# Optimization experiments

Hardware: AMD Instinct MI355X
Metric: run time of the kernel (lower is better)

## Reference

```python
import jax, jax.numpy as jnp
import numpy as np

N, E, F_IN = 50000, 1_600_000, 256
HID, HEADS, NCLS = 8, 8, 16  # conv1: 8 heads x 8 dims (concat=64); conv2: 1 head -> 16 classes


def setup_inputs() -> dict:
    key = jax.random.key(0)
    ks = jax.random.split(key, 11)
    x = jax.random.normal(ks[0], (N, F_IN), dtype=jnp.float32)
    edge_index = jax.random.randint(ks[1], (2, E), 0, N, dtype=jnp.int32)
    s1 = 1.0 / np.sqrt(F_IN)
    W1 = jax.random.normal(ks[2], (F_IN, HEADS * HID), jnp.float32) * s1
    a_src1 = jax.random.normal(ks[3], (HEADS, HID), jnp.float32) * 0.1
    a_dst1 = jax.random.normal(ks[4], (HEADS, HID), jnp.float32) * 0.1
    b1 = jnp.zeros((HEADS * HID,), jnp.float32)
    s2 = 1.0 / np.sqrt(HEADS * HID)
    W2 = jax.random.normal(ks[5], (HEADS * HID, NCLS), jnp.float32) * s2
    a_src2 = jax.random.normal(ks[6], (1, NCLS), jnp.float32) * 0.1
    a_dst2 = jax.random.normal(ks[7], (1, NCLS), jnp.float32) * 0.1
    b2 = jnp.zeros((NCLS,), jnp.float32)
    return {"x": x, "edge_index": edge_index, "W1": W1, "a_src1": a_src1,
            "a_dst1": a_dst1, "b1": b1, "W2": W2, "a_src2": a_src2,
            "a_dst2": a_dst2, "b2": b2}


def _gat_conv(x, W, a_src, a_dst, bias, src, dst, n, heads, ch, concat):
    # per-head linear transform: [n, heads, ch]
    h = (x @ W).reshape(n, heads, ch)
    # additive attention logits per node, per head
    al_s = jnp.einsum('nhc,hc->nh', h, a_src)
    al_d = jnp.einsum('nhc,hc->nh', h, a_dst)
    e = jax.nn.leaky_relu(al_s[src] + al_d[dst], 0.2)  # [E_tot, heads]
    # segment softmax grouped by destination node (self-loops guarantee non-empty segments)
    m = jax.ops.segment_max(e, dst, num_segments=n)
    ex = jnp.exp(e - m[dst])
    den = jax.ops.segment_sum(ex, dst, num_segments=n)
    alpha = ex / den[dst]  # [E_tot, heads]
    # scatter-aggregate weighted neighbor features
    out = jax.ops.segment_sum(h[src] * alpha[:, :, None], dst, num_segments=n)
    out = out.reshape(n, heads * ch) if concat else out.mean(axis=1)
    return out + bias


def reference(x, edge_index, W1, a_src1, a_dst1, b1, W2, a_src2, a_dst2, b2):
    # add self-loops (PyG GATConv default)
    loops = jnp.arange(N, dtype=edge_index.dtype)
    src = jnp.concatenate([edge_index[0], loops])
    dst = jnp.concatenate([edge_index[1], loops])
    h = _gat_conv(x, W1, a_src1, a_dst1, b1, src, dst, N, HEADS, HID, True)
    h = jax.nn.elu(h)
    out = _gat_conv(h, W2, a_src2, a_dst2, b2, src, dst, N, 1, NCLS, False)
    return jax.nn.log_softmax(out, axis=1)
```

## Files before the change

### kernel.cpp

```cpp
#include <hip/hip_runtime.h>
#include <hip/hip_fp16.h>

#define NN   50000
#define FIN  256
#define C1   64
#define NH   8
#define NC   16
#define NE   1600000
#define NTOT (NE + NN)

#define CH   256
#define EPC  ((NTOT + CH - 1) / CH)
#define NCB  392
#define GB1  ((NN + 63) / 64)

typedef _Float16 half8 __attribute__((ext_vector_type(8)));
typedef _Float16 half4 __attribute__((ext_vector_type(4)));
typedef float f32x4 __attribute__((ext_vector_type(4)));

#define OFF_H1H   0
#define OFF_G1H   1600000
#define OFF_STAGE 3200000
#define OFF_H2H   3200000
#define OFF_ALS2  3600000
#define OFF_ALD2  3650000
#define OFF_ALS1  6400000
#define OFF_ALD1  6800000
#define OFF_HM    7200000
#define OFF_BASEK 7300352
#define OFF_BBASE 7400704
#define OFF_OFFS  7401600
#define OFF_SRC   7451700
#define OFF_W1T   9101700

__global__ __launch_bounds__(256) void k_wcvt(const float* __restrict__ W1,
                                              _Float16* __restrict__ w1t) {
    int t = blockIdx.x * 256 + threadIdx.x;
    int c = t >> 8, k = t & 255;
    w1t[t] = (_Float16)W1[k * C1 + c];
}

__global__ __launch_bounds__(256) void k_g1rh(const float* __restrict__ x,
                                              const _Float16* __restrict__ w1t,
                                              const float* __restrict__ as1,
                                              const float* __restrict__ ad1,
                                              _Float16* __restrict__ h1h,
                                              float* __restrict__ als,
                                              float* __restrict__ ald,
                                              const int* __restrict__ ei,
                                              int* __restrict__ H) {
    __shared__ _Float16 wsT[64][264];
    __shared__ int lh[NCB];
    const int tid = threadIdx.x;

    if (blockIdx.x >= GB1) {
        int k = blockIdx.x - GB1;
        for (int i = tid; i < NCB; i += 256) lh[i] = 0;
        __syncthreads();
        int e0 = k * EPC, e1 = min(e0 + EPC, NTOT);
        for (int e = e0 + tid; e < e1; e += 256) {
            int d = (e < NE) ? ei[NE + e] : (e - NE);
            atomicAdd(&lh[d >> 7], 1);
        }
        __syncthreads();
        for (int i = tid; i < NCB; i += 256) H[k * NCB + i] = lh[i];
        return;
    }

    const int r0 = blockIdx.x * 64;
    #pragma unroll
    for (int j = 0; j < 8; ++j) {
        int idx = tid * 8 + j * 2048;
        int c = idx >> 8, ko = idx & 255;
        *(half8*)(&wsT[c][ko]) = *(const half8*)(&w1t[idx]);
    }
    __syncthreads();

    const int lane = tid & 63;
    const int wv   = tid >> 6;
    const int colb = lane & 15;
    const int rgrp = lane >> 4;
    const int arow = r0 + wv * 16 + colb;
    const bool arv = arow < NN;
    f32x4 acc[4] = {};
    #pragma unroll
    for (int s = 0; s < 8; ++s) {
        float4 v0 = make_float4(0.f,0.f,0.f,0.f), v1 = v0;
        if (arv) {
            const float4* xp = (const float4*)(&x[(size_t)arow * FIN + s * 32 + rgrp * 8]);
            v0 = xp[0]; v1 = xp[1];
        }
        half8 a;
        a[0]=(_Float16)v0.x; a[1]=(_Float16)v0.y; a[2]=(_Float16)v0.z; a[3]=(_Float16)v0.w;
        a[4]=(_Float16)v1.x; a[5]=(_Float16)v1.y; a[6]=(_Float16)v1.z; a[7]=(_Float16)v1.w;
        #pragma unroll
        for (int ct = 0; ct < 4; ++ct) {
            half8 b = *(half8*)(&wsT[ct * 16 + colb][s * 32 + rgrp * 8]);
            acc[ct] = __builtin_amdgcn_mfma_f32_16x16x32_f16(a, b, acc[ct], 0, 0, 0);
        }
    }
    __syncthreads();
    _Float16 (*hstore)[72] = (_Float16(*)[72])wsT;
    #pragma unroll
    for (int j = 0; j < 4; ++j) {
        int row = wv * 16 + rgrp * 4 + j;
        #pragma unroll
        for (int ct = 0; ct < 4; ++ct)
            hstore[row][ct * 16 + colb] = (_Float16)acc[ct][j];
    }
    __syncthreads();
    {
        int row = tid >> 2, seg = tid & 3;
        int grow = r0 + row;
        if (grow < NN) {
            half8 h0 = *(half8*)(&hstore[row][seg * 16]);
            half8 h1v = *(half8*)(&hstore[row][seg * 16 + 8]);
            *(half8*)(&h1h[(size_t)grow * C1 + seg * 16])     = h0;
            *(half8*)(&h1h[(size_t)grow * C1 + seg * 16 + 8]) = h1v;
            float ps0 = 0.f, pd0 = 0.f, ps1 = 0.f, pd1 = 0.f;
            #pragma unroll
            for (int u = 0; u < 8; ++u) {
                float a0 = (float)h0[u], a1 = (float)h1v[u];
                ps0 += a0 * as1[seg * 16 + u];
                pd0 += a0 * ad1[seg * 16 + u];
                ps1 += a1 * as1[seg * 16 + 8 + u];
                pd1 += a1 * ad1[seg * 16 + 8 + u];
            }
            als[grow * NH + seg * 2]     = ps0;
            als[grow * NH + seg * 2 + 1] = ps1;
            ald[grow * NH + seg * 2]     = pd0;
            ald[grow * NH + seg * 2 + 1] = pd1;
        }
    }
}

__global__ __launch_bounds__(256) void k_rsA(const int* __restrict__ H,
                                             int* __restrict__ basek,
                                             int* __restrict__ btot) {
    __shared__ int sc[CH];
    int b = blockIdx.x, t = threadIdx.x;
    int v = H[t * NCB + b];
    sc[t] = v;
    __syncthreads();
    for (int s = 1; s < CH; s <<= 1) {
        int u = (t >= s) ? sc[t - s] : 0;
        __syncthreads();
        sc[t] += u;
        __syncthreads();
    }
    basek[b * CH + t] = sc[t] - v;
    if (t == CH - 1) btot[b] = sc[t];
}

__global__ __launch_bounds__(512) void k_rsB(const int* __restrict__ btot,
                                             int* __restrict__ bbase,
                                             int* __restrict__ offs) {
    __shared__ int sc[512];
    int t = threadIdx.x;
    int v = (t < NCB) ? btot[t] : 0;
    sc[t] = v;
    __syncthreads();
    for (int s = 1; s < 512; s <<= 1) {
        int u = (t >= s) ? sc[t - s] : 0;
        __syncthreads();
        sc[t] += u;
        __syncthreads();
    }
    if (t < NCB) bbase[t] = sc[t] - v;
    if (t == NCB - 1) bbase[NCB] = sc[t];
    if (t == 0) offs[NN] = NTOT;
}

__global__ __launch_bounds__(256) void k_rscatter(const int* __restrict__ ei,
                                                  const int* __restrict__ basek,
                                                  const int* __restrict__ bbase,
                                                  int* __restrict__ stage) {
    __shared__ int lcur[NCB];
    int k = blockIdx.x;
    for (int i = threadIdx.x; i < NCB; i += 256)
        lcur[i] = bbase[i] + basek[i * CH + k];
    __syncthreads();
    int e0 = k * EPC, e1 = min(e0 + EPC, NTOT);
    for (int e = e0 + threadIdx.x; e < e1; e += 256) {
        int s, d;
        if (e < NE) { s = ei[e]; d = ei[NE + e]; }
        else        { s = e - NE; d = s; }
        int pos = atomicAdd(&lcur[d >> 7], 1);
        stage[pos] = (s << 7) | (d & 127);
    }
}

__global__ __launch_bounds__(256) void k_fsort(const int* __restrict__ stage,
                                               const int* __restrict__ bbase,
                                               int* __restrict__ offs,
                                               int* __restrict__ ssrc) {
    __shared__ int lc[128];
    __shared__ int ls[128];
    __shared__ int lcur[128];
    int b = blockIdx.x, t = threadIdx.x;
    int base = bbase[b];
    int n = bbase[b + 1] - base;
    if (t < 128) lc[t] = 0;
    __syncthreads();
    const int* sp = &stage[base];
    for (int i = t; i < n; i += 256) atomicAdd(&lc[sp[i] & 127], 1);
    __syncthreads();
    int v = (t < 128) ? lc[t] : 0;
    if (t < 128) ls[t] = v;
    __syncthreads();
    for (int s = 1; s < 128; s <<= 1) {
        int u = (t >= s && t < 128) ? ls[t - s] : 0;
        __syncthreads();
        if (t < 128) ls[t] += u;
        __syncthreads();
    }
    if (t < 128) {
        int excl = ls[t] - v;
        int d = b * 128 + t;
        if (d < NN) offs[d] = base + excl;
        lcur[t] = base + excl;
    }
    __syncthreads();
    for (int i = t; i < n; i += 256) {
        int u = sp[i];
        int pos = atomicAdd(&lcur[u & 127], 1);
        ssrc[pos] = u >> 7;
    }
}

__global__ __launch_bounds__(256) void k_agg1(const int* __restrict__ offs,
                                              const int* __restrict__ src,
                                              const __half* __restrict__ h1h,
                                              const float* __restrict__ als,
                                              const float* __restrict__ ald,
                                              const float* __restrict__ b1,
                                              _Float16* __restrict__ g1h) {
    int d = blockIdx.x * 4 + (threadIdx.x >> 6);
    if (d >= NN) return;
    const int l  = threadIdx.x & 63;
    const int q  = l >> 4, lc = l & 15;
    const int hg = lc >> 1;
    const int sub = l >> 3, hw = l & 7;
    const int lane_a = (q << 3) | hg;
    const int lane_b = lane_a + 32;
    const unsigned coff = (unsigned)lc * 8u;
    const unsigned hoff = (unsigned)hw * 4u;
    const char* h1b = (const char*)h1h;
    const char* alb = (const char*)als;
    int beg = offs[d], end = offs[d + 1];
    float aldv = ald[d * NH + hw];
    f32x4 acc = {0.f, 0.f, 0.f, 0.f};
    float wsum = 0.f;

    int r = beg;
    int e0 = r + sub, e1 = e0 + 8;
    int s0 = src[e0 < end ? e0 : end - 1];
    int s1 = src[e1 < end ? e1 : end - 1];
    {
        float lg0 = *(const float*)(alb + ((unsigned)s0 * 32u + hoff)) + aldv;
        float lg1 = *(const float*)(alb + ((unsigned)s1 * 32u + hoff)) + aldv;
        lg0 = lg0 > 0.f ? lg0 : 0.2f * lg0;
        lg1 = lg1 > 0.f ? lg1 : 0.2f * lg1;
        s0 = e0 < end ? s0 : s0;
        float w0t = e0 < end ? __expf(lg0) : 0.f;
        float w1t = e1 < end ? __expf(lg1) : 0.f;
        acc[0] = acc[0];
        float w0 = w0t, w1 = w1t;
        while (r < end) {
            int rn = r + 16;
            bool more = rn < end;
            int s0n = s0, s1n = s1;
            if (more) {
                int f0 = rn + sub, f1 = f0 + 8;
                s0n = src[f0 < end ? f0 : end - 1];
                s1n = src[f1 < end ? f1 : end - 1];
            }
            wsum += w0 + w1;
            #pragma unroll
            for (int i = 0; i < 4; ++i) {
                int srcl = (i & 1) ? lane_b : lane_a;
                int sv   = __shfl((i < 2) ? s0 : s1, srcl);
                float wv = __shfl((i < 2) ? w0 : w1, srcl);
                half4 hv = *(const half4*)(h1b + ((unsigned)sv * 128u + coff));
                acc[0] += wv * (float)hv[0];
                acc[1] += wv * (float)hv[1];
                acc[2] += wv * (float)hv[2];
                acc[3] += wv * (float)hv[3];
            }
            if (more) {
                float g0 = *(const float*)(alb + ((unsigned)s0n * 32u + hoff)) + aldv;
                float g1 = *(const float*)(alb + ((unsigned)s1n * 32u + hoff)) + aldv;
                g0 = g0 > 0.f ? g0 : 0.2f * g0;
                g1 = g1 > 0.f ? g1 : 0.2f * g1;
                w0 = (rn + sub) < end ? __expf(g0) : 0.f;
                w1 = (rn + 8 + sub) < end ? __expf(g1) : 0.f;
            }
            s0 = s0n; s1 = s1n; r = rn;
        }
    }
    #pragma unroll
    for (int k = 0; k < 4; ++k) {
        acc[k] += __shfl_xor(acc[k], 16);
        acc[k] += __shfl_xor(acc[k], 32);
    }
    wsum += __shfl_xor(wsum, 8);
    wsum += __shfl_xor(wsum, 16);
    wsum += __shfl_xor(wsum, 32);
    float den = __shfl(wsum, hg);
    if (q == 0) {
        half4 gv;
        #pragma unroll
        for (int k = 0; k < 4; ++k) {
            float o = acc[k] / den + b1[4 * lc + k];
            o = o > 0.f ? o : (__expf(o) - 1.f);
            gv[k] = (_Float16)o;
        }
        *(half4*)(&g1h[(size_t)d * C1 + 4 * lc]) = gv;
    }
}

__global__ __launch_bounds__(256) void k_gemm2(const _Float16* __restrict__ g1h,
                                               const float* __restrict__ W2,
                                               const float* __restrict__ as2,
                                               const float* __restrict__ ad2,
                                               _Float16* __restrict__ h2h,
                                               float* __restrict__ als2,
                                               float* __restrict__ ald2) {
    __shared__ float w2s[C1][17];
    __shared__ _Float16 hact[16][C1 + 8];
    int tid = threadIdx.x;
    for (int i = tid; i < C1 * NC; i += 256) w2s[i >> 4][i & 15] = W2[i];
    int ln = tid >> 4, j = tid & 15;
    int n = blockIdx.x * 16 + ln;
    if (n < NN)
        *(half4*)(&hact[ln][j * 4]) = *(const half4*)(&g1h[(size_t)n * C1 + j * 4]);
    __syncthreads();
    if (n >= NN) return;
    float sum = 0.f;
    #pragma unroll
    for (int c = 0; c < C1; ++c) sum += (float)hact[ln][c] * w2s[c][j];
    h2h[(size_t)n * NC + j] = (_Float16)sum;
    float ps = sum * as2[j], pd = sum * ad2[j];
    #pragma unroll
    for (int w = 1; w < 16; w <<= 1) {
        ps += __shfl_xor(ps, w);
        pd += __shfl_xor(pd, w);
    }
    if (j == 0) { als2[n] = ps; ald2[n] = pd; }
}

__global__ __launch_bounds__(256) void k_agg2(const int* __restrict__ offs,
                                              const int* __restrict__ src,
                                              const _Float16* __restrict__ h2h,
                                              const float* __restrict__ als2,
                                              const float* __restrict__ ald2,
                                              const float* __restrict__ b2,
                                              float* __restrict__ out) {
    int d = blockIdx.x * 16 + (threadIdx.x >> 4);
    if (d >= NN) return;
    int c = threadIdx.x & 15;
    const unsigned coff = (unsigned)c * 2u;
    const char* h2b = (const char*)h2h;
    const char* alb = (const char*)als2;
    int beg = offs[d], end = offs[d + 1];
    float aldv = ald2[d];
    float acc = 0.f, den = 0.f;
    for (int r = beg; r < end; r += 8) {
        int ss[8];
        float ww[8];
        #pragma unroll
        for (int i = 0; i < 8; ++i) {
            int e = r + i;
            ss[i] = src[e < end ? e : end - 1];
        }
        #pragma unroll
        for (int i = 0; i < 8; ++i) {
            float lg = *(const float*)(alb + (unsigned)ss[i] * 4u) + aldv;
            lg = lg > 0.f ? lg : 0.2f * lg;
            ww[i] = (r + i) < end ? __expf(lg) : 0.f;
        }
        #pragma unroll
        for (int i = 0; i < 8; ++i) {
            float hv = (float)*(const _Float16*)(h2b + ((unsigned)ss[i] * 32u + coff));
            acc += ww[i] * hv;
            den += ww[i];
        }
    }
    float o = acc / den + b2[c];
    float m = o;
    #pragma unroll
    for (int w = 1; w < 16; w <<= 1) m = fmaxf(m, __shfl_xor(m, w));
    float ex = __expf(o - m);
    float sm = ex;
    #pragma unroll
    for (int w = 1; w < 16; w <<= 1) sm += __shfl_xor(sm, w);
    out[(size_t)d * NC + c] = o - m - __logf(sm);
}

extern "C" void kernel_launch(void* const* d_in, const int* in_sizes, int n_in,
                              void* d_out, int out_size, void* d_ws, size_t ws_size,
                              hipStream_t stream) {
    const float* x   = (const float*)d_in[0];
    const int*   ei  = (const int*)  d_in[1];
    const float* W1  = (const float*)d_in[2];
    const float* as1 = (const float*)d_in[3];
    const float* ad1 = (const float*)d_in[4];
    const float* b1  = (const float*)d_in[5];
    const float* W2  = (const float*)d_in[6];
    const float* as2 = (const float*)d_in[7];
    const float* ad2 = (const float*)d_in[8];
    const float* b2  = (const float*)d_in[9];
    float* ws  = (float*)d_ws;
    float* out = (float*)d_out;

    _Float16*  h1h  = (_Float16*)(ws + OFF_H1H);
    _Float16*  g1h  = (_Float16*)(ws + OFF_G1H);
    _Float16*  h2h  = (_Float16*)(ws + OFF_H2H);
    _Float16*  w1t  = (_Float16*)(ws + OFF_W1T);
    float* als1 = ws + OFF_ALS1;
    float* ald1 = ws + OFF_ALD1;
    float* als2 = ws + OFF_ALS2;
    float* ald2 = ws + OFF_ALD2;
    int* H      = (int*)(ws + OFF_HM);
    int* basek  = (int*)(ws + OFF_BASEK);
    int* bbase  = (int*)(ws + OFF_BBASE);
    int* btot   = (int*)(ws + OFF_BBASE) + 400;
    int* offs   = (int*)(ws + OFF_OFFS);
    int* ssrc   = (int*)(ws + OFF_SRC);
    int* stage  = (int*)(ws + OFF_STAGE);

    k_wcvt    <<<64,             256, 0, stream>>>(W1, w1t);
    k_g1rh    <<<GB1 + CH,       256, 0, stream>>>(x, w1t, as1, ad1, h1h, als1, ald1, ei, H);
    k_rsA     <<<NCB,            256, 0, stream>>>(H, basek, btot);
    k_rsB     <<<1,              512, 0, stream>>>(btot, bbase, offs);
    k_rscatter<<<CH,             256, 0, stream>>>(ei, basek, bbase, stage);
    k_fsort   <<<NCB,            256, 0, stream>>>(stage, bbase, offs, ssrc);
    k_agg1    <<<(NN + 3) / 4,   256, 0, stream>>>(offs, ssrc, (const __half*)h1h, als1, ald1, b1, g1h);
    k_gemm2   <<<(NN + 15) / 16, 256, 0, stream>>>(g1h, W2, as2, ad2, h2h, als2, ald2);
    k_agg2    <<<(NN + 15) / 16, 256, 0, stream>>>(offs, ssrc, h2h, als2, ald2, b2, out);
}
```

Measured before the change: 137.4 us.

## Drop W1 convert and rsB kernels, widen sort buckets, restructure aggregation kernels

Removes the separate W1 fp16 transpose kernel by converting W1 inline when loading shared memory in the GEMM, and folds the single-block bucket-total scan into the scatter and fine-sort kernels, which each recompute it. Bucket width doubles from 128 to 256 nodes, halving the bucket count. Layer-1 aggregation now gives each lane its own edge slot with half8 feature loads instead of shuffle-based broadcasting and software prefetch. Layer-2 aggregation uses a 64-lane wave per node with half4 loads and float4 output stores. Fewer launches and wider memory ops are traded for redundant scans and uncoalesced W1 reads per GEMM block.

```diff
diff --git a/kernel.cpp b/kernel.cpp
--- a/kernel.cpp
+++ b/kernel.cpp
@@ -11,7 +11,7 @@
 
 #define CH   256
 #define EPC  ((NTOT + CH - 1) / CH)
-#define NCB  392
+#define NCB  196
 #define GB1  ((NN + 63) / 64)
 
 typedef _Float16 half8 __attribute__((ext_vector_type(8)));
@@ -28,20 +28,12 @@
 #define OFF_ALD1  6800000
 #define OFF_HM    7200000
 #define OFF_BASEK 7300352
-#define OFF_BBASE 7400704
+#define OFF_BTOT  7400704
 #define OFF_OFFS  7401600
 #define OFF_SRC   7451700
-#define OFF_W1T   9101700
-
-__global__ __launch_bounds__(256) void k_wcvt(const float* __restrict__ W1,
-                                              _Float16* __restrict__ w1t) {
-    int t = blockIdx.x * 256 + threadIdx.x;
-    int c = t >> 8, k = t & 255;
-    w1t[t] = (_Float16)W1[k * C1 + c];
-}
 
 __global__ __launch_bounds__(256) void k_g1rh(const float* __restrict__ x,
-                                              const _Float16* __restrict__ w1t,
+                                              const float* __restrict__ W1,
                                               const float* __restrict__ as1,
                                               const float* __restrict__ ad1,
                                               _Float16* __restrict__ h1h,
@@ -60,7 +52,7 @@
         int e0 = k * EPC, e1 = min(e0 + EPC, NTOT);
         for (int e = e0 + tid; e < e1; e += 256) {
             int d = (e < NE) ? ei[NE + e] : (e - NE);
-            atomicAdd(&lh[d >> 7], 1);
+            atomicAdd(&lh[d >> 8], 1);
         }
         __syncthreads();
         for (int i = tid; i < NCB; i += 256) H[k * NCB + i] = lh[i];
@@ -68,11 +60,17 @@
     }
 
     const int r0 = blockIdx.x * 64;
-    #pragma unroll
-    for (int j = 0; j < 8; ++j) {
-        int idx = tid * 8 + j * 2048;
-        int c = idx >> 8, ko = idx & 255;
-        *(half8*)(&wsT[c][ko]) = *(const half8*)(&w1t[idx]);
+    {
+        int c = tid & 63, kb = tid >> 6;
+        #pragma unroll
+        for (int j = 0; j < 8; ++j) {
+            int k8 = kb + 4 * j;
+            half8 hv;
+            #pragma unroll
+            for (int u = 0; u < 8; ++u)
+                hv[u] = (_Float16)W1[(size_t)(k8 * 8 + u) * C1 + c];
+            *(half8*)(&wsT[c][k8 * 8]) = hv;
+        }
     }
     __syncthreads();
 
@@ -152,170 +150,140 @@
     if (t == CH - 1) btot[b] = sc[t];
 }
 
-__global__ __launch_bounds__(512) void k_rsB(const int* __restrict__ btot,
-                                             int* __restrict__ bbase,
-                                             int* __restrict__ offs) {
-    __shared__ int sc[512];
-    int t = threadIdx.x;
+__global__ __launch_bounds__(256) void k_rscatter(const int* __restrict__ ei,
+                                                  const int* __restrict__ basek,
+                                                  const int* __restrict__ btot,
+                                                  int* __restrict__ stage) {
+    __shared__ int sc[256];
+    __shared__ int lcur[NCB];
+    int k = blockIdx.x, t = threadIdx.x;
     int v = (t < NCB) ? btot[t] : 0;
     sc[t] = v;
     __syncthreads();
-    for (int s = 1; s < 512; s <<= 1) {
+    for (int s = 1; s < 256; s <<= 1) {
         int u = (t >= s) ? sc[t - s] : 0;
         __syncthreads();
         sc[t] += u;
         __syncthreads();
     }
-    if (t < NCB) bbase[t] = sc[t] - v;
-    if (t == NCB - 1) bbase[NCB] = sc[t];
-    if (t == 0) offs[NN] = NTOT;
-}
-
-__global__ __launch_bounds__(256) void k_rscatter(const int* __restrict__ ei,
-                                                  const int* __restrict__ basek,
-                                                  const int* __restrict__ bbase,
-                                                  int* __restrict__ stage) {
-    __shared__ int lcur[NCB];
-    int k = blockIdx.x;
-    for (int i = threadIdx.x; i < NCB; i += 256)
-        lcur[i] = bbase[i] + basek[i * CH + k];
+    if (t < NCB) lcur[t] = (sc[t] - v) + basek[t * CH + k];
     __syncthreads();
     int e0 = k * EPC, e1 = min(e0 + EPC, NTOT);
-    for (int e = e0 + threadIdx.x; e < e1; e += 256) {
+    for (int e = e0 + t; e < e1; e += 256) {
         int s, d;
         if (e < NE) { s = ei[e]; d = ei[NE + e]; }
         else        { s = e - NE; d = s; }
-        int pos = atomicAdd(&lcur[d >> 7], 1);
-        stage[pos] = (s << 7) | (d & 127);
+        int pos = atomicAdd(&lcur[d >> 8], 1);
+        stage[pos] = (s << 8) | (d & 255);
     }
 }
 
 __global__ __launch_bounds__(256) void k_fsort(const int* __restrict__ stage,
-                                               const int* __restrict__ bbase,
+                                               const int* __restrict__ btot,
                                                int* __restrict__ offs,
                                                int* __restrict__ ssrc) {
-    __shared__ int lc[128];
-    __shared__ int ls[128];
-    __shared__ int lcur[128];
+    __shared__ int sc[256];
+    __shared__ int lc[256];
+    __shared__ int ls[256];
+    __shared__ int lcur[256];
+    __shared__ int bb[2];
     int b = blockIdx.x, t = threadIdx.x;
-    int base = bbase[b];
-    int n = bbase[b + 1] - base;
-    if (t < 128) lc[t] = 0;
-    __syncthreads();
+    int v = (t < NCB) ? btot[t] : 0;
+    sc[t] = v;
+    __syncthreads();
+    for (int s = 1; s < 256; s <<= 1) {
+        int u = (t >= s) ? sc[t - s] : 0;
+        __syncthreads();
+        sc[t] += u;
+        __syncthreads();
+    }
+    if (t == b) bb[0] = sc[t] - v;
+    if (t == b) bb[1] = sc[t];
+    if (b == 0 && t == 0) offs[NN] = NTOT;
+    lc[t] = 0;
+    __syncthreads();
+    int base = bb[0];
+    int n = bb[1] - base;
     const int* sp = &stage[base];
-    for (int i = t; i < n; i += 256) atomicAdd(&lc[sp[i] & 127], 1);
-    __syncthreads();
-    int v = (t < 128) ? lc[t] : 0;
-    if (t < 128) ls[t] = v;
-    __syncthreads();
-    for (int s = 1; s < 128; s <<= 1) {
-        int u = (t >= s && t < 128) ? ls[t - s] : 0;
-        __syncthreads();
-        if (t < 128) ls[t] += u;
-        __syncthreads();
-    }
-    if (t < 128) {
-        int excl = ls[t] - v;
-        int d = b * 128 + t;
-        if (d < NN) offs[d] = base + excl;
-        lcur[t] = base + excl;
-    }
+    for (int i = t; i < n; i += 256) atomicAdd(&lc[sp[i] & 255], 1);
+    __syncthreads();
+    int hv = lc[t];
+    ls[t] = hv;
+    __syncthreads();
+    for (int s = 1; s < 256; s <<= 1) {
+        int u = (t >= s) ? ls[t - s] : 0;
+        __syncthreads();
+        ls[t] += u;
+        __syncthreads();
+    }
+    int excl = ls[t] - hv;
+    int d = b * 256 + t;
+    if (d < NN) offs[d] = base + excl;
+    lcur[t] = base + excl;
     __syncthreads();
     for (int i = t; i < n; i += 256) {
         int u = sp[i];
-        int pos = atomicAdd(&lcur[u & 127], 1);
-        ssrc[pos] = u >> 7;
+        int pos = atomicAdd(&lcur[u & 255], 1);
+        ssrc[pos] = u >> 8;
     }
 }
 
 __global__ __launch_bounds__(256) void k_agg1(const int* __restrict__ offs,
                                               const int* __restrict__ src,
-                                              const __half* __restrict__ h1h,
+                                              const _Float16* __restrict__ h1h,
                                               const float* __restrict__ als,
                                               const float* __restrict__ ald,
                                               const float* __restrict__ b1,
                                               _Float16* __restrict__ g1h) {
     int d = blockIdx.x * 4 + (threadIdx.x >> 6);
     if (d >= NN) return;
-    const int l  = threadIdx.x & 63;
-    const int q  = l >> 4, lc = l & 15;
-    const int hg = lc >> 1;
-    const int sub = l >> 3, hw = l & 7;
-    const int lane_a = (q << 3) | hg;
-    const int lane_b = lane_a + 32;
-    const unsigned coff = (unsigned)lc * 8u;
-    const unsigned hoff = (unsigned)hw * 4u;
+    const int l = threadIdx.x & 63;
+    const int slot = l >> 3, hd = l & 7;
+    const unsigned hoff = (unsigned)hd * 4u;
+    const unsigned coff = (unsigned)hd * 16u;
+    const char* alb = (const char*)als;
     const char* h1b = (const char*)h1h;
-    const char* alb = (const char*)als;
     int beg = offs[d], end = offs[d + 1];
-    float aldv = ald[d * NH + hw];
-    f32x4 acc = {0.f, 0.f, 0.f, 0.f};
+    float aldv = ald[d * NH + hd];
+    float acc[8] = {};
     float wsum = 0.f;
 
-    int r = beg;
-    int e0 = r + sub, e1 = e0 + 8;
-    int s0 = src[e0 < end ? e0 : end - 1];
-    int s1 = src[e1 < end ? e1 : end - 1];
-    {
+    for (int r = beg; r < end; r += 16) {
+        int e0 = r + slot, e1 = e0 + 8;
+        bool v0 = e0 < end, v1 = e1 < end;
+        int s0 = src[v0 ? e0 : end - 1];
+        int s1 = src[v1 ? e1 : end - 1];
+        half8 h0 = *(const half8*)(h1b + ((unsigned)s0 * 128u + coff));
+        half8 h1v = *(const half8*)(h1b + ((unsigned)s1 * 128u + coff));
         float lg0 = *(const float*)(alb + ((unsigned)s0 * 32u + hoff)) + aldv;
         float lg1 = *(const float*)(alb + ((unsigned)s1 * 32u + hoff)) + aldv;
         lg0 = lg0 > 0.f ? lg0 : 0.2f * lg0;
         lg1 = lg1 > 0.f ? lg1 : 0.2f * lg1;
-        s0 = e0 < end ? s0 : s0;
-        float w0t = e0 < end ? __expf(lg0) : 0.f;
-        float w1t = e1 < end ? __expf(lg1) : 0.f;
-        acc[0] = acc[0];
-        float w0 = w0t, w1 = w1t;
-        while (r < end) {
-            int rn = r + 16;
-            bool more = rn < end;
-            int s0n = s0, s1n = s1;
-            if (more) {
-                int f0 = rn + sub, f1 = f0 + 8;
-                s0n = src[f0 < end ? f0 : end - 1];
-                s1n = src[f1 < end ? f1 : end - 1];
-            }
-            wsum += w0 + w1;
-            #pragma unroll
-            for (int i = 0; i < 4; ++i) {
-                int srcl = (i & 1) ? lane_b : lane_a;
-                int sv   = __shfl((i < 2) ? s0 : s1, srcl);
-                float wv = __shfl((i < 2) ? w0 : w1, srcl);
-                half4 hv = *(const half4*)(h1b + ((unsigned)sv * 128u + coff));
-                acc[0] += wv * (float)hv[0];
-                acc[1] += wv * (float)hv[1];
-                acc[2] += wv * (float)hv[2];
-                acc[3] += wv * (float)hv[3];
-            }
-            if (more) {
-                float g0 = *(const float*)(alb + ((unsigned)s0n * 32u + hoff)) + aldv;
-                float g1 = *(const float*)(alb + ((unsigned)s1n * 32u + hoff)) + aldv;
-                g0 = g0 > 0.f ? g0 : 0.2f * g0;
-                g1 = g1 > 0.f ? g1 : 0.2f * g1;
-                w0 = (rn + sub) < end ? __expf(g0) : 0.f;
-                w1 = (rn + 8 + sub) < end ? __expf(g1) : 0.f;
-            }
-            s0 = s0n; s1 = s1n; r = rn;
-        }
-    }
-    #pragma unroll
-    for (int k = 0; k < 4; ++k) {
-        acc[k] += __shfl_xor(acc[k], 16);
-        acc[k] += __shfl_xor(acc[k], 32);
+        float w0 = v0 ? __expf(lg0) : 0.f;
+        float w1 = v1 ? __expf(lg1) : 0.f;
+        wsum += w0 + w1;
+        #pragma unroll
+        for (int u = 0; u < 8; ++u)
+            acc[u] += w0 * (float)h0[u] + w1 * (float)h1v[u];
+    }
+    #pragma unroll
+    for (int u = 0; u < 8; ++u) {
+        acc[u] += __shfl_xor(acc[u], 8);
+        acc[u] += __shfl_xor(acc[u], 16);
+        acc[u] += __shfl_xor(acc[u], 32);
     }
     wsum += __shfl_xor(wsum, 8);
     wsum += __shfl_xor(wsum, 16);
     wsum += __shfl_xor(wsum, 32);
-    float den = __shfl(wsum, hg);
-    if (q == 0) {
-        half4 gv;
-        #pragma unroll
-        for (int k = 0; k < 4; ++k) {
-            float o = acc[k] / den + b1[4 * lc + k];
+    if (slot == 0) {
+        half8 gv;
+        #pragma unroll
+        for (int u = 0; u < 8; ++u) {
+            float o = acc[u] / wsum + b1[hd * 8 + u];
             o = o > 0.f ? o : (__expf(o) - 1.f);
-            gv[k] = (_Float16)o;
-        }
-        *(half4*)(&g1h[(size_t)d * C1 + 4 * lc]) = gv;
+            gv[u] = (_Float16)o;
+        }
+        *(half8*)(&g1h[(size_t)d * C1 + hd * 8]) = gv;
     }
 }
 
@@ -356,45 +324,60 @@
                                               const float* __restrict__ ald2,
                                               const float* __restrict__ b2,
                                               float* __restrict__ out) {
-    int d = blockIdx.x * 16 + (threadIdx.x >> 4);
+    int d = blockIdx.x * 4 + (threadIdx.x >> 6);
     if (d >= NN) return;
-    int c = threadIdx.x & 15;
-    const unsigned coff = (unsigned)c * 2u;
+    const int l = threadIdx.x & 63;
+    const int slot = l >> 2, cq = l & 3;
+    const unsigned coff = (unsigned)cq * 8u;
     const char* h2b = (const char*)h2h;
     const char* alb = (const char*)als2;
     int beg = offs[d], end = offs[d + 1];
     float aldv = ald2[d];
-    float acc = 0.f, den = 0.f;
-    for (int r = beg; r < end; r += 8) {
-        int ss[8];
-        float ww[8];
-        #pragma unroll
-        for (int i = 0; i < 8; ++i) {
-            int e = r + i;
-            ss[i] = src[e < end ? e : end - 1];
-        }
-        #pragma unroll
-        for (int i = 0; i < 8; ++i) {
-            float lg = *(const float*)(alb + (unsigned)ss[i] * 4u) + aldv;
-            lg = lg > 0.f ? lg : 0.2f * lg;
-            ww[i] = (r + i) < end ? __expf(lg) : 0.f;
-        }
-        #pragma unroll
-        for (int i = 0; i < 8; ++i) {
-            float hv = (float)*(const _Float16*)(h2b + ((unsigned)ss[i] * 32u + coff));
-            acc += ww[i] * hv;
-            den += ww[i];
-        }
-    }
-    float o = acc / den + b2[c];
-    float m = o;
-    #pragma unroll
-    for (int w = 1; w < 16; w <<= 1) m = fmaxf(m, __shfl_xor(m, w));
-    float ex = __expf(o - m);
-    float sm = ex;
-    #pragma unroll
-    for (int w = 1; w < 16; w <<= 1) sm += __shfl_xor(sm, w);
-    out[(size_t)d * NC + c] = o - m - __logf(sm);
+    float acc[4] = {};
+    float wsum = 0.f;
+    for (int r = beg; r < end; r += 16) {
+        int e = r + slot;
+        bool v = e < end;
+        int s = src[v ? e : end - 1];
+        half4 hv = *(const half4*)(h2b + ((unsigned)s * 32u + coff));
+        float lg = *(const float*)(alb + (unsigned)s * 4u) + aldv;
+        lg = lg > 0.f ? lg : 0.2f * lg;
+        float w = v ? __expf(lg) : 0.f;
+        wsum += w;
+        #pragma unroll
+        for (int u = 0; u < 4; ++u)
+            acc[u] += w * (float)hv[u];
+    }
+    #pragma unroll
+    for (int u = 0; u < 4; ++u) {
+        acc[u] += __shfl_xor(acc[u], 4);
+        acc[u] += __shfl_xor(acc[u], 8);
+        acc[u] += __shfl_xor(acc[u], 16);
+        acc[u] += __shfl_xor(acc[u], 32);
+    }
+    wsum += __shfl_xor(wsum, 4);
+    wsum += __shfl_xor(wsum, 8);
+    wsum += __shfl_xor(wsum, 16);
+    wsum += __shfl_xor(wsum, 32);
+    float o[4];
+    float m = -1e30f;
+    #pragma unroll
+    for (int u = 0; u < 4; ++u) {
+        o[u] = acc[u] / wsum + b2[cq * 4 + u];
+        m = fmaxf(m, o[u]);
+    }
+    m = fmaxf(m, __shfl_xor(m, 1));
+    m = fmaxf(m, __shfl_xor(m, 2));
+    float sm = 0.f;
+    #pragma unroll
+    for (int u = 0; u < 4; ++u) sm += __expf(o[u] - m);
+    sm += __shfl_xor(sm, 1);
+    sm += __shfl_xor(sm, 2);
+    float lse = m + __logf(sm);
+    if (slot == 0) {
+        float4 ov = make_float4(o[0] - lse, o[1] - lse, o[2] - lse, o[3] - lse);
+        *(float4*)(&out[(size_t)d * NC + cq * 4]) = ov;
+    }
 }
 
 extern "C" void kernel_launch(void* const* d_in, const int* in_sizes, int n_in,
@@ -416,26 +399,22 @@
     _Float16*  h1h  = (_Float16*)(ws + OFF_H1H);
     _Float16*  g1h  = (_Float16*)(ws + OFF_G1H);
     _Float16*  h2h  = (_Float16*)(ws + OFF_H2H);
-    _Float16*  w1t  = (_Float16*)(ws + OFF_W1T);
     float* als1 = ws + OFF_ALS1;
     float* ald1 = ws + OFF_ALD1;
     float* als2 = ws + OFF_ALS2;
     float* ald2 = ws + OFF_ALD2;
     int* H      = (int*)(ws + OFF_HM);
     int* basek  = (int*)(ws + OFF_BASEK);
-    int* bbase  = (int*)(ws + OFF_BBASE);
-    int* btot   = (int*)(ws + OFF_BBASE) + 400;
+    int* btot   = (int*)(ws + OFF_BTOT);
     int* offs   = (int*)(ws + OFF_OFFS);
     int* ssrc   = (int*)(ws + OFF_SRC);
     int* stage  = (int*)(ws + OFF_STAGE);
 
-    k_wcvt    <<<64,             256, 0, stream>>>(W1, w1t);
-    k_g1rh    <<<GB1 + CH,       256, 0, stream>>>(x, w1t, as1, ad1, h1h, als1, ald1, ei, H);
+    k_g1rh    <<<GB1 + CH,       256, 0, stream>>>(x, W1, as1, ad1, h1h, als1, ald1, ei, H);
     k_rsA     <<<NCB,            256, 0, stream>>>(H, basek, btot);
-    k_rsB     <<<1,              512, 0, stream>>>(btot, bbase, offs);
-    k_rscatter<<<CH,             256, 0, stream>>>(ei, basek, bbase, stage);
-    k_fsort   <<<NCB,            256, 0, stream>>>(stage, bbase, offs, ssrc);
-    k_agg1    <<<(NN + 3) / 4,   256, 0, stream>>>(offs, ssrc, (const __half*)h1h, als1, ald1, b1, g1h);
+    k_rscatter<<<CH,             256, 0, stream>>>(ei, basek, btot, stage);
+    k_fsort   <<<NCB,            256, 0, stream>>>(stage, btot, offs, ssrc);
+    k_agg1    <<<(NN + 3) / 4,   256, 0, stream>>>(offs, ssrc, h1h, als1, ald1, b1, g1h);
     k_gemm2   <<<(NN + 15) / 16, 256, 0, stream>>>(g1h, W2, as2, ad2, h2h, als2, ald2);
-    k_agg2    <<<(NN + 15) / 16, 256, 0, stream>>>(offs, ssrc, h2h, als2, ald2, b2, out);
-}
+    k_agg2    <<<(NN + 3) / 4,   256, 0, stream>>>(offs, ssrc, h2h, als2, ald2, b2, out);
+}
```

After: 135.9 us. Within noise of the previous version (-1.1%).
